# Optimization experiments

Measured on AMD Instinct MI355X. Metric: run time of the kernel, lower is better.

The kernel has to match this reference:

```python
import jax, jax.numpy as jnp
import numpy as np

D_MODEL = 768
N_HEADS = 12
HEAD_DIM = D_MODEL // N_HEADS
D_FF = 4 * D_MODEL
EPS = 1e-5


def setup_inputs() -> dict:
    key = jax.random.key(0)
    ks = jax.random.split(key, 16)
    s = 0.02
    x = jax.random.normal(ks[0], (2, 2048, D_MODEL), dtype=jnp.float32)
    wq = jax.random.normal(ks[1], (D_MODEL, D_MODEL), dtype=jnp.float32) * s
    bq = jnp.zeros((D_MODEL,), jnp.float32)
    wk = jax.random.normal(ks[2], (D_MODEL, D_MODEL), dtype=jnp.float32) * s
    bk = jnp.zeros((D_MODEL,), jnp.float32)
    wv = jax.random.normal(ks[3], (D_MODEL, D_MODEL), dtype=jnp.float32) * s
    bv = jnp.zeros((D_MODEL,), jnp.float32)
    wo = jax.random.normal(ks[4], (D_MODEL, D_MODEL), dtype=jnp.float32) * s
    bo = jnp.zeros((D_MODEL,), jnp.float32)
    w1 = jax.random.normal(ks[5], (D_MODEL, D_FF), dtype=jnp.float32) * s
    b1 = jnp.zeros((D_FF,), jnp.float32)
    w2 = jax.random.normal(ks[6], (D_FF, D_MODEL), dtype=jnp.float32) * s
    b2 = jnp.zeros((D_MODEL,), jnp.float32)
    ln1_g = jnp.ones((D_MODEL,), jnp.float32)
    ln1_b = jnp.zeros((D_MODEL,), jnp.float32)
    ln2_g = jnp.ones((D_MODEL,), jnp.float32)
    ln2_b = jnp.zeros((D_MODEL,), jnp.float32)
    return dict(x=x, wq=wq, bq=bq, wk=wk, bk=bk, wv=wv, bv=bv, wo=wo, bo=bo,
                w1=w1, b1=b1, w2=w2, b2=b2,
                ln1_g=ln1_g, ln1_b=ln1_b, ln2_g=ln2_g, ln2_b=ln2_b)


def _layernorm(x, g, b):
    mu = jnp.mean(x, axis=-1, keepdims=True)
    var = jnp.mean(jnp.square(x - mu), axis=-1, keepdims=True)
    return (x - mu) * jax.lax.rsqrt(var + EPS) * g + b


def _attention(x, wq, bq, wk, bk, wv, bv, wo, bo):
    B, S, D = x.shape
    def split_heads(t):  # [B,S,D] -> [B,H,S,Hd]
        return t.reshape(B, S, N_HEADS, HEAD_DIM).transpose(0, 2, 1, 3)
    q = split_heads(x @ wq + bq)
    k = split_heads(x @ wk + bk)
    v = split_heads(x @ wv + bv)
    scores = jnp.einsum('bhqd,bhkd->bhqk', q, k) / np.sqrt(HEAD_DIM).astype(np.float32)
    causal = jnp.tril(jnp.ones((S, S), dtype=bool))
    scores = jnp.where(causal, scores, -jnp.inf)
    weights = jax.nn.softmax(scores, axis=-1)
    attn = jnp.einsum('bhqk,bhkd->bhqd', weights, v)
    attn = attn.transpose(0, 2, 1, 3).reshape(B, S, D)
    return attn @ wo + bo


def reference(x, wq, bq, wk, bk, wv, bv, wo, bo, w1, b1, w2, b2,
              ln1_g, ln1_b, ln2_g, ln2_b):
    x = x + _attention(_layernorm(x, ln1_g, ln1_b), wq, bq, wk, bk, wv, bv, wo, bo)
    h = _layernorm(x, ln2_g, ln2_b)
    ff = jax.nn.relu(h @ w1 + b1) @ w2 + b2
    return x + ff
```

## Files before the change

### kernel.cpp

```cpp
#include <hip/hip_runtime.h>
#include <stdint.h>

typedef __bf16 bf16;
typedef float f32x4 __attribute__((ext_vector_type(4)));
typedef bf16 bf16x8 __attribute__((ext_vector_type(8)));
typedef bf16 bf16x4 __attribute__((ext_vector_type(4)));

#define MFMA16(a, b, c) __builtin_amdgcn_mfma_f32_16x16x32_bf16((a), (b), (c), 0, 0, 0)

static __device__ __forceinline__ void load_lds16(const bf16* g, bf16* l) {
  __builtin_amdgcn_global_load_lds(
      (const __attribute__((address_space(1))) void*)g,
      (__attribute__((address_space(3))) void*)l, 16, 0, 0);
}

static __device__ __forceinline__ void xcd_swz(int& bx, int& by, int& bz) {
  int gx = gridDim.x, gy = gridDim.y;
  int lin = blockIdx.x + gx * (blockIdx.y + gy * blockIdx.z);
  int nwg = gx * gy * gridDim.z;
  int nl = (lin & 7) * (nwg >> 3) + (lin >> 3);
  bx = nl % gx;
  int t = nl / gx;
  by = t % gy;
  bz = t / gy;
}

__global__ void __launch_bounds__(256) k_prep(
    const float* __restrict__ x, const float* __restrict__ ln1g,
    const float* __restrict__ ln1b, bf16* __restrict__ h1,
    const float* s0, const float* s1, const float* s2, const float* s3,
    const float* s4, const float* s5,
    bf16* d0, bf16* d1, bf16* d2, bf16* d3, bf16* d4, bf16* d5) {
  int t = blockIdx.x;
  int tid = threadIdx.x;
  if (t < 6912) {
    const float* src; bf16* dst; int R, C;
    if (t < 2304) {
      int z = t / 576; t -= z * 576;
      src = (z == 0) ? s0 : (z == 1) ? s1 : (z == 2) ? s2 : s3;
      dst = (z == 0) ? d0 : (z == 1) ? d1 : (z == 2) ? d2 : d3;
      R = 768; C = 768;
    } else if (t < 4608) {
      t -= 2304; src = s4; dst = d4; R = 768; C = 3072;
    } else {
      t -= 4608; src = s5; dst = d5; R = 3072; C = 768;
    }
    int tcn = C >> 5;
    int tr = t / tcn, tc = t % tcn;
    __shared__ float tile[32][33];
    int tx = tid & 31, ty = tid >> 5;
    for (int i = 0; i < 4; i++)
      tile[ty + i * 8][tx] = src[(size_t)(tr * 32 + ty + i * 8) * C + tc * 32 + tx];
    __syncthreads();
    for (int i = 0; i < 4; i++)
      dst[(size_t)(tc * 32 + ty + i * 8) * R + tr * 32 + tx] = (bf16)tile[tx][ty + i * 8];
  } else {
    int row = t - 6912;
    const float* rp = x + (size_t)row * 768;
    float v0 = rp[tid], v1 = rp[tid + 256], v2 = rp[tid + 512];
    float s = v0 + v1 + v2, sq = v0 * v0 + v1 * v1 + v2 * v2;
    for (int off = 1; off < 64; off <<= 1) {
      s += __shfl_xor(s, off, 64);
      sq += __shfl_xor(sq, off, 64);
    }
    __shared__ float ps[8];
    if ((tid & 63) == 0) { ps[tid >> 6] = s; ps[4 + (tid >> 6)] = sq; }
    __syncthreads();
    s = ps[0] + ps[1] + ps[2] + ps[3];
    sq = ps[4] + ps[5] + ps[6] + ps[7];
    float mu = s * (1.0f / 768.0f);
    float rstd = rsqrtf(sq * (1.0f / 768.0f) - mu * mu + 1e-5f);
    bf16* op = h1 + (size_t)row * 768;
    op[tid] = (bf16)((v0 - mu) * rstd * ln1g[tid] + ln1b[tid]);
    op[tid + 256] = (bf16)((v1 - mu) * rstd * ln1g[tid + 256] + ln1b[tid + 256]);
    op[tid + 512] = (bf16)((v2 - mu) * rstd * ln1g[tid + 512] + ln1b[tid + 512]);
  }
}

__global__ void __launch_bounds__(256) k_ln2_reduce(
    const float* __restrict__ p0, const float* __restrict__ p1,
    const float* __restrict__ x, const float* __restrict__ bo,
    const float* __restrict__ gam, const float* __restrict__ bet,
    float* __restrict__ x1, bf16* __restrict__ h2) {
  int row = blockIdx.x, tid = threadIdx.x;
  size_t base = (size_t)row * 768;
  float v0 = p0[base + tid] + p1[base + tid] + x[base + tid] + bo[tid];
  float v1 = p0[base + tid + 256] + p1[base + tid + 256] + x[base + tid + 256] + bo[tid + 256];
  float v2 = p0[base + tid + 512] + p1[base + tid + 512] + x[base + tid + 512] + bo[tid + 512];
  x1[base + tid] = v0; x1[base + tid + 256] = v1; x1[base + tid + 512] = v2;
  float s = v0 + v1 + v2, sq = v0 * v0 + v1 * v1 + v2 * v2;
  for (int off = 1; off < 64; off <<= 1) {
    s += __shfl_xor(s, off, 64);
    sq += __shfl_xor(sq, off, 64);
  }
  __shared__ float ps[8];
  if ((tid & 63) == 0) { ps[tid >> 6] = s; ps[4 + (tid >> 6)] = sq; }
  __syncthreads();
  s = ps[0] + ps[1] + ps[2] + ps[3];
  sq = ps[4] + ps[5] + ps[6] + ps[7];
  float mu = s * (1.0f / 768.0f);
  float rstd = rsqrtf(sq * (1.0f / 768.0f) - mu * mu + 1e-5f);
  bf16* op = h2 + base;
  op[tid] = (bf16)((v0 - mu) * rstd * gam[tid] + bet[tid]);
  op[tid + 256] = (bf16)((v1 - mu) * rstd * gam[tid + 256] + bet[tid + 256]);
  op[tid + 512] = (bf16)((v2 - mu) * rstd * gam[tid + 512] + bet[tid + 512]);
}

__global__ void __launch_bounds__(256) k_ff2_reduce(
    const float* __restrict__ f0, const float* __restrict__ f1,
    const float* __restrict__ x1, const float* __restrict__ b2,
    float* __restrict__ out) {
  size_t i = ((size_t)blockIdx.x * 256 + threadIdx.x) * 4;
  int col = (int)(i % 768);
  f32x4 v = *(const f32x4*)(x1 + i);
  f32x4 b = *(const f32x4*)(b2 + col);
  f32x4 a0 = *(const f32x4*)(f0 + i), a1 = *(const f32x4*)(f1 + i);
  *(f32x4*)(out + i) = v + b + a0 + a1;
}

template <int MT>
static __device__ __forceinline__ void gemm_core(
    const bf16* __restrict__ A, int lda, const bf16* __restrict__ Bt, int ldb,
    int Kc, int m0, int n0, bf16* As, bf16* Bs, f32x4 acc[MT][4]) {
  int tid = threadIdx.x, w = tid >> 6, lane = tid & 63, quad = lane >> 4, l15 = lane & 15;
  int wr = w >> 1, wc = w & 1;
  int srow = lane >> 2;
  int sk = (((lane & 3) ^ ((srow >> 1) & 3)) * 8);
  int rsw = ((l15 >> 1) & 3);
  const int ABUF = MT * 32 * 32;
  const int BBUF = 128 * 32;

  auto stage = [&](int k0, int buf) {
    bf16* Ab = As + buf * ABUF;
    bf16* Bb = Bs + buf * BBUF;
    if (MT == 4) {
      for (int c = 0; c < 2; c++) {
        int seg = w * 2 + c;
        load_lds16(A + (size_t)(m0 + seg * 16 + srow) * lda + k0 + sk, Ab + seg * 512);
      }
    } else {
      load_lds16(A + (size_t)(m0 + w * 16 + srow) * lda + k0 + sk, Ab + w * 512);
    }
    for (int c = 0; c < 2; c++) {
      int seg = w * 2 + c;
      load_lds16(Bt + (size_t)(n0 + seg * 16 + srow) * ldb + k0 + sk, Bb + seg * 512);
    }
  };

  stage(0, 0);
  stage(32, 1);
  int cur = 0;
  for (int k0 = 0; k0 < Kc; k0 += 32) {
    if (k0 + 32 < Kc) {
      if (MT == 4) asm volatile("s_waitcnt vmcnt(4)" ::: "memory");
      else         asm volatile("s_waitcnt vmcnt(3)" ::: "memory");
    } else {
      asm volatile("s_waitcnt vmcnt(0)" ::: "memory");
    }
    __builtin_amdgcn_s_barrier();
    __builtin_amdgcn_sched_barrier(0);
    if (k0 + 64 < Kc) {
      int nb = cur + 2; if (nb >= 3) nb -= 3;
      stage(k0 + 64, nb);
    }
    const bf16* Ab = As + cur * ABUF;
    const bf16* Bb = Bs + cur * BBUF;
    bf16x8 af[MT], bfr[4];
    for (int mi = 0; mi < MT; mi++)
      af[mi] = *(const bf16x8*)(Ab + (wr * (MT * 16) + mi * 16 + l15) * 32 + ((quad ^ rsw) * 8));
    for (int ni = 0; ni < 4; ni++)
      bfr[ni] = *(const bf16x8*)(Bb + (wc * 64 + ni * 16 + l15) * 32 + ((quad ^ rsw) * 8));
    for (int mi = 0; mi < MT; mi++)
      for (int ni = 0; ni < 4; ni++)
        acc[mi][ni] = MFMA16(af[mi], bfr[ni], acc[mi][ni]);
    cur = cur + 1; if (cur >= 3) cur -= 3;
  }
}

template <int MT>
static __device__ __forceinline__ void gemm_core64(
    const bf16* __restrict__ A, int lda, const bf16* __restrict__ Bt, int ldb,
    int Kc, int m0, int n0, bf16* As, bf16* Bs, f32x4 acc[MT][4]) {
  int tid = threadIdx.x, w = tid >> 6, lane = tid & 63, quad = lane >> 4, l15 = lane & 15;
  int wr = w >> 1, wc = w & 1;
  int srow = lane >> 2;
  int sk = (((lane & 3) ^ ((srow >> 1) & 3)) * 8);
  int rsw = ((l15 >> 1) & 3);
  const int ASUB = MT * 32 * 32;
  const int BSUB = 128 * 32;
  const int ABUF = 2 * ASUB;
  const int BBUF = 2 * BSUB;

  auto stage = [&](int k0, int buf) {
    bf16* Ab = As + buf * ABUF;
    bf16* Bb = Bs + buf * BBUF;
    for (int h = 0; h < 2; h++) {
      if (MT == 4) {
        for (int c = 0; c < 2; c++) {
          int seg = w * 2 + c;
          load_lds16(A + (size_t)(m0 + seg * 16 + srow) * lda + k0 + h * 32 + sk,
                     Ab + h * ASUB + seg * 512);
        }
      } else {
        load_lds16(A + (size_t)(m0 + w * 16 + srow) * lda + k0 + h * 32 + sk,
                   Ab + h * ASUB + w * 512);
      }
      for (int c = 0; c < 2; c++) {
        int seg = w * 2 + c;
        load_lds16(Bt + (size_t)(n0 + seg * 16 + srow) * ldb + k0 + h * 32 + sk,
                   Bb + h * BSUB + seg * 512);
      }
    }
  };

  stage(0, 0);
  int cur = 0;
  for (int k0 = 0; k0 < Kc; k0 += 64) {
    __syncthreads();
    if (k0 + 64 < Kc) stage(k0 + 64, cur ^ 1);
    const bf16* Ab = As + cur * ABUF;
    const bf16* Bb = Bs + cur * BBUF;
    for (int h = 0; h < 2; h++) {
      bf16x8 af[MT], bfr[4];
      for (int mi = 0; mi < MT; mi++)
        af[mi] = *(const bf16x8*)(Ab + h * ASUB +
                 (wr * (MT * 16) + mi * 16 + l15) * 32 + ((quad ^ rsw) * 8));
      for (int ni = 0; ni < 4; ni++)
        bfr[ni] = *(const bf16x8*)(Bb + h * BSUB +
                  (wc * 64 + ni * 16 + l15) * 32 + ((quad ^ rsw) * 8));
      for (int mi = 0; mi < MT; mi++)
        for (int ni = 0; ni < 4; ni++)
          acc[mi][ni] = MFMA16(af[mi], bfr[ni], acc[mi][ni]);
    }
    cur ^= 1;
  }
}

template <int MT>
__global__ void __launch_bounds__(256, 3) k_gemm(
    const bf16* __restrict__ A, const bf16* __restrict__ Bt,
    const float* __restrict__ bias, bf16* __restrict__ outp, int K_, int N_) {
  __shared__ __align__(16) bf16 As[3 * MT * 32 * 32];
  __shared__ __align__(16) bf16 Bs[3 * 128 * 32];
  int bx, by, bz;
  xcd_swz(bx, by, bz);
  int m0 = by * (MT * 32), n0 = bx * 128;
  f32x4 acc[MT][4] = {};
  gemm_core<MT>(A, K_, Bt, K_, K_, m0, n0, As, Bs, acc);
  int tid = threadIdx.x, w = tid >> 6, lane = tid & 63, quad = lane >> 4, l15 = lane & 15;
  int wr = w >> 1, wc = w & 1;
  float bv[4];
  for (int ni = 0; ni < 4; ni++) bv[ni] = bias[n0 + wc * 64 + ni * 16 + l15];
  for (int mi = 0; mi < MT; mi++) {
    int mb = m0 + wr * (MT * 16) + mi * 16 + quad * 4;
    for (int ni = 0; ni < 4; ni++) {
      int n = n0 + wc * 64 + ni * 16 + l15;
      for (int r = 0; r < 4; r++) {
        float val = acc[mi][ni][r] + bv[ni];
        outp[(size_t)(mb + r) * N_ + n] = (bf16)fmaxf(val, 0.0f);
      }
    }
  }
}

__global__ void __launch_bounds__(256, 3) k_gemm_split64(
    const bf16* __restrict__ A, const bf16* __restrict__ Bt,
    float* __restrict__ f0, float* __restrict__ f1, int K_, int Kc, int N_) {
  __shared__ __align__(16) bf16 As[2 * 2 * 2 * 32 * 32];
  __shared__ __align__(16) bf16 Bs[2 * 2 * 128 * 32];
  int bx, by, bz;
  xcd_swz(bx, by, bz);
  float* outp = (bz == 0) ? f0 : f1;
  int m0 = by * 64, n0 = bx * 128;
  f32x4 acc[2][4] = {};
  gemm_core64<2>(A + (size_t)bz * Kc, K_, Bt + (size_t)bz * Kc, K_, Kc, m0, n0, As, Bs, acc);
  int tid = threadIdx.x, w = tid >> 6, lane = tid & 63, quad = lane >> 4, l15 = lane & 15;
  int wr = w >> 1, wc = w & 1;
  for (int mi = 0; mi < 2; mi++) {
    int mb = m0 + wr * 32 + mi * 16 + quad * 4;
    for (int ni = 0; ni < 4; ni++) {
      int n = n0 + wc * 64 + ni * 16 + l15;
      for (int r = 0; r < 4; r++)
        outp[(size_t)(mb + r) * N_ + n] = acc[mi][ni][r];
    }
  }
}

__global__ void __launch_bounds__(256, 3) k_gemm_qkv64(
    const bf16* __restrict__ h1, const bf16* __restrict__ wqT,
    const bf16* __restrict__ wkT, const bf16* __restrict__ wvT,
    const float* __restrict__ bq, const float* __restrict__ bk,
    const float* __restrict__ bv, bf16* __restrict__ qb,
    bf16* __restrict__ kb, bf16* __restrict__ vtb) {
  __shared__ __align__(16) bf16 As[2 * 2 * 2 * 32 * 32];
  __shared__ __align__(16) bf16 Bs[2 * 2 * 128 * 32];
  int bx, by, bz;
  xcd_swz(bx, by, bz);
  int z = bz;
  const bf16* Bt = (z == 0) ? wqT : (z == 1) ? wkT : wvT;
  const float* bias = (z == 0) ? bq : (z == 1) ? bk : bv;
  int m0 = by * 64, n0 = bx * 128;
  f32x4 acc[2][4] = {};
  gemm_core64<2>(h1, 768, Bt, 768, 768, m0, n0, As, Bs, acc);
  int tid = threadIdx.x, w = tid >> 6, lane = tid & 63, quad = lane >> 4, l15 = lane & 15;
  int wr = w >> 1, wc = w & 1;
  float bvv[4];
  for (int ni = 0; ni < 4; ni++) bvv[ni] = bias[n0 + wc * 64 + ni * 16 + l15];
  for (int mi = 0; mi < 2; mi++) {
    int mb = m0 + wr * 32 + mi * 16 + quad * 4;
    int b = mb >> 11, s0_ = mb & 2047;
    for (int ni = 0; ni < 4; ni++) {
      int n = n0 + wc * 64 + ni * 16 + l15;
      int h = n >> 6, hd = n & 63;
      if (z < 2) {
        bf16* outp = (z == 0) ? qb : kb;
        size_t base = (size_t)(b * 12 + h) * 2048 * 64;
        for (int r = 0; r < 4; r++)
          outp[base + (size_t)(s0_ + r) * 64 + hd] = (bf16)(acc[mi][ni][r] + bvv[ni]);
      } else {
        bf16x4 pk;
        for (int r = 0; r < 4; r++) pk[r] = (bf16)(acc[mi][ni][r] + bvv[ni]);
        *(bf16x4*)(vtb + (((size_t)(b * 12 + h) * 64 + hd) * 2048 + s0_)) = pk;
      }
    }
  }
}

__global__ void __launch_bounds__(256, 2) k_attn(
    const bf16* __restrict__ qb, const bf16* __restrict__ kb,
    const bf16* __restrict__ vtb, bf16* __restrict__ out) {
  __shared__ __align__(16) bf16 Ks[2 * 128 * 64];
  __shared__ __align__(16) bf16 Vs[2 * 64 * 128];
  __shared__ __align__(16) bf16 Ps[4][16 * 128];
  int qt = 31 - (blockIdx.x / 24);
  int bh = blockIdx.x % 24;
  int q0 = qt * 64;
  int tid = threadIdx.x, w = tid >> 6, lane = tid & 63, quad = lane >> 4, l15 = lane & 15;
  const bf16* qbase = qb + (size_t)bh * 2048 * 64;
  const bf16* kbase = kb + (size_t)bh * 2048 * 64;
  const bf16* vbase = vtb + (size_t)bh * 64 * 2048;

  bf16x8 qf[2];
  for (int ds = 0; ds < 2; ds++)
    qf[ds] = *(const bf16x8*)(qbase + (size_t)(q0 + w * 16 + l15) * 64 + ds * 32 + quad * 8);

  bf16 one_ = (bf16)1.0f;
  bf16x8 ones8 = {one_, one_, one_, one_, one_, one_, one_, one_};

  f32x4 o[4] = {};
  f32x4 lacc = {};

  auto stageKV = [&](int k0, int buf) {
    int rsub = lane >> 3, c8 = lane & 7;
    bf16* Kb = Ks + buf * (128 * 64);
    for (int c = 0; c < 4; c++) {
      int seg = c * 4 + w;
      int row = seg * 8 + rsub;
      load_lds16(kbase + (size_t)(k0 + row) * 64 + ((c8 ^ (row & 7)) * 8), Kb + seg * 512);
    }
    int rsub2 = lane >> 4, c16 = lane & 15;
    bf16* Vb = Vs + buf * (64 * 128);
    for (int c = 0; c < 4; c++) {
      int seg = c * 4 + w;
      int row = seg * 4 + rsub2;
      load_lds16(vbase + (size_t)row * 2048 + k0 + ((c16 ^ (row & 15)) * 8), Vb + seg * 512);
    }
  };

  const float C2 = 0.18033688011112042f;
  int nkt = (qt >> 1) + 1;
  stageKV(0, 0);
  int cur = 0;
  for (int kt = 0; kt < nkt; kt++) {
    int k0 = kt * 128;
    __syncthreads();
    if (kt + 1 < nkt) stageKV(k0 + 128, cur ^ 1);
    const bf16* Kb = Ks + cur * (128 * 64);
    const bf16* Vb = Vs + cur * (64 * 128);

    f32x4 sc[8] = {};
    __builtin_amdgcn_s_setprio(1);
    for (int kj = 0; kj < 8; kj++) {
      int krow = kj * 16 + l15;
      for (int ds = 0; ds < 2; ds++) {
        bf16x8 kf = *(const bf16x8*)(Kb + krow * 64 + (((ds * 4 + quad) ^ (krow & 7)) * 8));
        sc[kj] = MFMA16(qf[ds], kf, sc[kj]);
      }
    }
    __builtin_amdgcn_s_setprio(0);
    if (kt == nkt - 1) {
      int qg = q0 + w * 16 + quad * 4;
      for (int kj = 0; kj < 8; kj++) {
        int kg = k0 + kj * 16 + l15;
        for (int r = 0; r < 4; r++)
          if (kg > qg + r) sc[kj][r] = -3.0e38f;
      }
    }
    for (int kj = 0; kj < 8; kj++)
      for (int r = 0; r < 4; r++)
        sc[kj][r] = exp2f(sc[kj][r] * C2);
    for (int kj = 0; kj < 8; kj++) {
      int colb = kj * 16 + l15;
      int chb = colb >> 3, cin = colb & 7;
      for (int r = 0; r < 4; r++) {
        int prow = quad * 4 + r;
        Ps[w][prow * 128 + ((chb ^ prow) * 8) + cin] = (bf16)sc[kj][r];
      }
    }
    __builtin_amdgcn_s_setprio(1);
    for (int ks = 0; ks < 4; ks++) {
      int prow = l15;
      bf16x8 pf = *(const bf16x8*)(&Ps[w][prow * 128 + (((ks * 4 + quad) ^ prow) * 8)]);
      lacc = MFMA16(pf, ones8, lacc);
      for (int dj = 0; dj < 4; dj++) {
        int vrow = dj * 16 + l15;
        bf16x8 vf = *(const bf16x8*)(Vb + vrow * 128 + (((ks * 4 + quad) ^ (vrow & 15)) * 8));
        o[dj] = MFMA16(pf, vf, o[dj]);
      }
    }
    __builtin_amdgcn_s_setprio(0);
    cur ^= 1;
  }
  int b = bh / 12, h = bh % 12;
  f32x4 rl;
  for (int r = 0; r < 4; r++) rl[r] = 1.0f / lacc[r];
  int srow = q0 + w * 16 + quad * 4;
  for (int dj = 0; dj < 4; dj++) {
    int d = h * 64 + dj * 16 + l15;
    for (int r = 0; r < 4; r++)
      out[(size_t)(b * 2048 + srow + r) * 768 + d] = (bf16)(o[dj][r] * rl[r]);
  }
}

extern "C" void kernel_launch(void* const* d_in, const int* in_sizes, int n_in,
                              void* d_out, int out_size, void* d_ws, size_t ws_size,
                              hipStream_t stream) {
  const float* x    = (const float*)d_in[0];
  const float* wq   = (const float*)d_in[1];
  const float* bq   = (const float*)d_in[2];
  const float* wk   = (const float*)d_in[3];
  const float* bk   = (const float*)d_in[4];
  const float* wv   = (const float*)d_in[5];
  const float* bv   = (const float*)d_in[6];
  const float* wo   = (const float*)d_in[7];
  const float* bo   = (const float*)d_in[8];
  const float* w1   = (const float*)d_in[9];
  const float* b1   = (const float*)d_in[10];
  const float* w2   = (const float*)d_in[11];
  const float* b2   = (const float*)d_in[12];
  const float* ln1g = (const float*)d_in[13];
  const float* ln1b = (const float*)d_in[14];
  const float* ln2g = (const float*)d_in[15];
  const float* ln2b = (const float*)d_in[16];

  char* p = (char*)d_ws;
  bf16* wqT = (bf16*)p; p += (size_t)768 * 768 * 2;
  bf16* wkT = (bf16*)p; p += (size_t)768 * 768 * 2;
  bf16* wvT = (bf16*)p; p += (size_t)768 * 768 * 2;
  bf16* woT = (bf16*)p; p += (size_t)768 * 768 * 2;
  bf16* w1T = (bf16*)p; p += (size_t)768 * 3072 * 2;
  bf16* w2T = (bf16*)p; p += (size_t)768 * 3072 * 2;
  bf16* h1   = (bf16*)p; p += (size_t)4096 * 768 * 2;
  bf16* qbuf = (bf16*)p; p += (size_t)4096 * 768 * 2;
  bf16* kbuf = (bf16*)p; p += (size_t)4096 * 768 * 2;
  bf16* vtb  = (bf16*)p; p += (size_t)4096 * 768 * 2;
  bf16* att  = (bf16*)p; p += (size_t)4096 * 768 * 2;
  float* x1  = (float*)p; p += (size_t)4096 * 768 * 4;
  bf16* h2   = (bf16*)p; p += (size_t)4096 * 768 * 2;
  bf16* ffm  = (bf16*)p; p += (size_t)4096 * 3072 * 2;
  float* p0  = (float*)p; p += (size_t)4096 * 768 * 4;
  float* p1  = (float*)p; p += (size_t)4096 * 768 * 4;
  float* f0 = (float*)h1;
  float* f1 = (float*)kbuf;

  k_prep<<<dim3(11008), dim3(256), 0, stream>>>(
      x, ln1g, ln1b, h1, wq, wk, wv, wo, w1, w2, wqT, wkT, wvT, woT, w1T, w2T);
  k_gemm_qkv64<<<dim3(6, 64, 3), dim3(256), 0, stream>>>(
      h1, wqT, wkT, wvT, bq, bk, bv, qbuf, kbuf, vtb);
  k_attn<<<dim3(768), dim3(256), 0, stream>>>(qbuf, kbuf, vtb, att);
  k_gemm_split64<<<dim3(6, 64, 2), dim3(256), 0, stream>>>(
      att, woT, p0, p1, 768, 384, 768);
  k_ln2_reduce<<<dim3(4096), dim3(256), 0, stream>>>(
      p0, p1, x, bo, ln2g, ln2b, x1, h2);
  k_gemm<4><<<dim3(24, 32), dim3(256), 0, stream>>>(
      h2, w1T, b1, ffm, 768, 3072);
  k_gemm_split64<<<dim3(6, 64, 2), dim3(256), 0, stream>>>(
      ffm, w2T, f0, f1, 3072, 1536, 768);
  k_ff2_reduce<<<dim3(3072), dim3(256), 0, stream>>>(
      f0, f1, x1, b2, (float*)d_out);
}
```

Baseline: 265.8 us.

## Fold residual into Wo GEMM, prescale Q, retile FF1 GEMM to 64-row

Moves the residual x and bias bo addition into the epilogue of the first split-K Wo GEMM partition, so the LN2 reduce kernel reads two fp32 arrays instead of four. Folds the softmax scale constant into Q when the QKV GEMM writes it, which removes one multiply per score in attention. Replaces the FF1 GEMM, which used a 128-row tile with a three-stage 32-K pipeline, with a 64-row tile using the double-buffered 64-K core. That doubles the grid and cuts per-block work. Rounding Q to bf16 after scaling changes numerics slightly.

After: 276.2 us. 1.04x slower.

```diff
diff --git a/kernel.cpp b/kernel.cpp
--- a/kernel.cpp
+++ b/kernel.cpp
@@ -79,14 +79,13 @@
 
 __global__ void __launch_bounds__(256) k_ln2_reduce(
     const float* __restrict__ p0, const float* __restrict__ p1,
-    const float* __restrict__ x, const float* __restrict__ bo,
     const float* __restrict__ gam, const float* __restrict__ bet,
     float* __restrict__ x1, bf16* __restrict__ h2) {
   int row = blockIdx.x, tid = threadIdx.x;
   size_t base = (size_t)row * 768;
-  float v0 = p0[base + tid] + p1[base + tid] + x[base + tid] + bo[tid];
-  float v1 = p0[base + tid + 256] + p1[base + tid + 256] + x[base + tid + 256] + bo[tid + 256];
-  float v2 = p0[base + tid + 512] + p1[base + tid + 512] + x[base + tid + 512] + bo[tid + 512];
+  float v0 = p0[base + tid] + p1[base + tid];
+  float v1 = p0[base + tid + 256] + p1[base + tid + 256];
+  float v2 = p0[base + tid + 512] + p1[base + tid + 512];
   x1[base + tid] = v0; x1[base + tid + 256] = v1; x1[base + tid + 512] = v2;
   float s = v0 + v1 + v2, sq = v0 * v0 + v1 * v1 + v2 * v2;
   for (int off = 1; off < 64; off <<= 1) {
@@ -118,75 +117,15 @@
   *(f32x4*)(out + i) = v + b + a0 + a1;
 }
 
-template <int MT>
-static __device__ __forceinline__ void gemm_core(
+static __device__ __forceinline__ void gemm_core64(
     const bf16* __restrict__ A, int lda, const bf16* __restrict__ Bt, int ldb,
-    int Kc, int m0, int n0, bf16* As, bf16* Bs, f32x4 acc[MT][4]) {
+    int Kc, int m0, int n0, bf16* As, bf16* Bs, f32x4 acc[2][4]) {
   int tid = threadIdx.x, w = tid >> 6, lane = tid & 63, quad = lane >> 4, l15 = lane & 15;
   int wr = w >> 1, wc = w & 1;
   int srow = lane >> 2;
   int sk = (((lane & 3) ^ ((srow >> 1) & 3)) * 8);
   int rsw = ((l15 >> 1) & 3);
-  const int ABUF = MT * 32 * 32;
-  const int BBUF = 128 * 32;
-
-  auto stage = [&](int k0, int buf) {
-    bf16* Ab = As + buf * ABUF;
-    bf16* Bb = Bs + buf * BBUF;
-    if (MT == 4) {
-      for (int c = 0; c < 2; c++) {
-        int seg = w * 2 + c;
-        load_lds16(A + (size_t)(m0 + seg * 16 + srow) * lda + k0 + sk, Ab + seg * 512);
-      }
-    } else {
-      load_lds16(A + (size_t)(m0 + w * 16 + srow) * lda + k0 + sk, Ab + w * 512);
-    }
-    for (int c = 0; c < 2; c++) {
-      int seg = w * 2 + c;
-      load_lds16(Bt + (size_t)(n0 + seg * 16 + srow) * ldb + k0 + sk, Bb + seg * 512);
-    }
-  };
-
-  stage(0, 0);
-  stage(32, 1);
-  int cur = 0;
-  for (int k0 = 0; k0 < Kc; k0 += 32) {
-    if (k0 + 32 < Kc) {
-      if (MT == 4) asm volatile("s_waitcnt vmcnt(4)" ::: "memory");
-      else         asm volatile("s_waitcnt vmcnt(3)" ::: "memory");
-    } else {
-      asm volatile("s_waitcnt vmcnt(0)" ::: "memory");
-    }
-    __builtin_amdgcn_s_barrier();
-    __builtin_amdgcn_sched_barrier(0);
-    if (k0 + 64 < Kc) {
-      int nb = cur + 2; if (nb >= 3) nb -= 3;
-      stage(k0 + 64, nb);
-    }
-    const bf16* Ab = As + cur * ABUF;
-    const bf16* Bb = Bs + cur * BBUF;
-    bf16x8 af[MT], bfr[4];
-    for (int mi = 0; mi < MT; mi++)
-      af[mi] = *(const bf16x8*)(Ab + (wr * (MT * 16) + mi * 16 + l15) * 32 + ((quad ^ rsw) * 8));
-    for (int ni = 0; ni < 4; ni++)
-      bfr[ni] = *(const bf16x8*)(Bb + (wc * 64 + ni * 16 + l15) * 32 + ((quad ^ rsw) * 8));
-    for (int mi = 0; mi < MT; mi++)
-      for (int ni = 0; ni < 4; ni++)
-        acc[mi][ni] = MFMA16(af[mi], bfr[ni], acc[mi][ni]);
-    cur = cur + 1; if (cur >= 3) cur -= 3;
-  }
-}
-
-template <int MT>
-static __device__ __forceinline__ void gemm_core64(
-    const bf16* __restrict__ A, int lda, const bf16* __restrict__ Bt, int ldb,
-    int Kc, int m0, int n0, bf16* As, bf16* Bs, f32x4 acc[MT][4]) {
-  int tid = threadIdx.x, w = tid >> 6, lane = tid & 63, quad = lane >> 4, l15 = lane & 15;
-  int wr = w >> 1, wc = w & 1;
-  int srow = lane >> 2;
-  int sk = (((lane & 3) ^ ((srow >> 1) & 3)) * 8);
-  int rsw = ((l15 >> 1) & 3);
-  const int ASUB = MT * 32 * 32;
+  const int ASUB = 2 * 32 * 32;
   const int BSUB = 128 * 32;
   const int ABUF = 2 * ASUB;
   const int BBUF = 2 * BSUB;
@@ -195,16 +134,8 @@
     bf16* Ab = As + buf * ABUF;
     bf16* Bb = Bs + buf * BBUF;
     for (int h = 0; h < 2; h++) {
-      if (MT == 4) {
-        for (int c = 0; c < 2; c++) {
-          int seg = w * 2 + c;
-          load_lds16(A + (size_t)(m0 + seg * 16 + srow) * lda + k0 + h * 32 + sk,
-                     Ab + h * ASUB + seg * 512);
-        }
-      } else {
-        load_lds16(A + (size_t)(m0 + w * 16 + srow) * lda + k0 + h * 32 + sk,
-                   Ab + h * ASUB + w * 512);
-      }
+      load_lds16(A + (size_t)(m0 + w * 16 + srow) * lda + k0 + h * 32 + sk,
+                 Ab + h * ASUB + w * 512);
       for (int c = 0; c < 2; c++) {
         int seg = w * 2 + c;
         load_lds16(Bt + (size_t)(n0 + seg * 16 + srow) * ldb + k0 + h * 32 + sk,
@@ -221,14 +152,14 @@
     const bf16* Ab = As + cur * ABUF;
     const bf16* Bb = Bs + cur * BBUF;
     for (int h = 0; h < 2; h++) {
-      bf16x8 af[MT], bfr[4];
-      for (int mi = 0; mi < MT; mi++)
+      bf16x8 af[2], bfr[4];
+      for (int mi = 0; mi < 2; mi++)
         af[mi] = *(const bf16x8*)(Ab + h * ASUB +
-                 (wr * (MT * 16) + mi * 16 + l15) * 32 + ((quad ^ rsw) * 8));
+                 (wr * 32 + mi * 16 + l15) * 32 + ((quad ^ rsw) * 8));
       for (int ni = 0; ni < 4; ni++)
         bfr[ni] = *(const bf16x8*)(Bb + h * BSUB +
                   (wc * 64 + ni * 16 + l15) * 32 + ((quad ^ rsw) * 8));
-      for (int mi = 0; mi < MT; mi++)
+      for (int mi = 0; mi < 2; mi++)
         for (int ni = 0; ni < 4; ni++)
           acc[mi][ni] = MFMA16(af[mi], bfr[ni], acc[mi][ni]);
     }
@@ -236,23 +167,22 @@
   }
 }
 
-template <int MT>
-__global__ void __launch_bounds__(256, 3) k_gemm(
+__global__ void __launch_bounds__(256, 3) k_gemm64(
     const bf16* __restrict__ A, const bf16* __restrict__ Bt,
     const float* __restrict__ bias, bf16* __restrict__ outp, int K_, int N_) {
-  __shared__ __align__(16) bf16 As[3 * MT * 32 * 32];
-  __shared__ __align__(16) bf16 Bs[3 * 128 * 32];
+  __shared__ __align__(16) bf16 As[2 * 2 * 2 * 32 * 32];
+  __shared__ __align__(16) bf16 Bs[2 * 2 * 128 * 32];
   int bx, by, bz;
   xcd_swz(bx, by, bz);
-  int m0 = by * (MT * 32), n0 = bx * 128;
-  f32x4 acc[MT][4] = {};
-  gemm_core<MT>(A, K_, Bt, K_, K_, m0, n0, As, Bs, acc);
+  int m0 = by * 64, n0 = bx * 128;
+  f32x4 acc[2][4] = {};
+  gemm_core64(A, K_, Bt, K_, K_, m0, n0, As, Bs, acc);
   int tid = threadIdx.x, w = tid >> 6, lane = tid & 63, quad = lane >> 4, l15 = lane & 15;
   int wr = w >> 1, wc = w & 1;
   float bv[4];
   for (int ni = 0; ni < 4; ni++) bv[ni] = bias[n0 + wc * 64 + ni * 16 + l15];
-  for (int mi = 0; mi < MT; mi++) {
-    int mb = m0 + wr * (MT * 16) + mi * 16 + quad * 4;
+  for (int mi = 0; mi < 2; mi++) {
+    int mb = m0 + wr * 32 + mi * 16 + quad * 4;
     for (int ni = 0; ni < 4; ni++) {
       int n = n0 + wc * 64 + ni * 16 + l15;
       for (int r = 0; r < 4; r++) {
@@ -265,7 +195,9 @@
 
 __global__ void __launch_bounds__(256, 3) k_gemm_split64(
     const bf16* __restrict__ A, const bf16* __restrict__ Bt,
-    float* __restrict__ f0, float* __restrict__ f1, int K_, int Kc, int N_) {
+    float* __restrict__ f0, float* __restrict__ f1,
+    const float* __restrict__ xadd, const float* __restrict__ badd,
+    int K_, int Kc, int N_) {
   __shared__ __align__(16) bf16 As[2 * 2 * 2 * 32 * 32];
   __shared__ __align__(16) bf16 Bs[2 * 2 * 128 * 32];
   int bx, by, bz;
@@ -273,15 +205,19 @@
   float* outp = (bz == 0) ? f0 : f1;
   int m0 = by * 64, n0 = bx * 128;
   f32x4 acc[2][4] = {};
-  gemm_core64<2>(A + (size_t)bz * Kc, K_, Bt + (size_t)bz * Kc, K_, Kc, m0, n0, As, Bs, acc);
+  gemm_core64(A + (size_t)bz * Kc, K_, Bt + (size_t)bz * Kc, K_, Kc, m0, n0, As, Bs, acc);
   int tid = threadIdx.x, w = tid >> 6, lane = tid & 63, quad = lane >> 4, l15 = lane & 15;
   int wr = w >> 1, wc = w & 1;
+  bool fold = (bz == 0) && (xadd != nullptr);
   for (int mi = 0; mi < 2; mi++) {
     int mb = m0 + wr * 32 + mi * 16 + quad * 4;
     for (int ni = 0; ni < 4; ni++) {
       int n = n0 + wc * 64 + ni * 16 + l15;
-      for (int r = 0; r < 4; r++)
-        outp[(size_t)(mb + r) * N_ + n] = acc[mi][ni][r];
+      for (int r = 0; r < 4; r++) {
+        float val = acc[mi][ni][r];
+        if (fold) val += xadd[(size_t)(mb + r) * N_ + n] + badd[n];
+        outp[(size_t)(mb + r) * N_ + n] = val;
+      }
     }
   }
 }
@@ -301,9 +237,11 @@
   const float* bias = (z == 0) ? bq : (z == 1) ? bk : bv;
   int m0 = by * 64, n0 = bx * 128;
   f32x4 acc[2][4] = {};
-  gemm_core64<2>(h1, 768, Bt, 768, 768, m0, n0, As, Bs, acc);
+  gemm_core64(h1, 768, Bt, 768, 768, m0, n0, As, Bs, acc);
   int tid = threadIdx.x, w = tid >> 6, lane = tid & 63, quad = lane >> 4, l15 = lane & 15;
   int wr = w >> 1, wc = w & 1;
+  const float C2 = 0.18033688011112042f;
+  float qs = (z == 0) ? C2 : 1.0f;
   float bvv[4];
   for (int ni = 0; ni < 4; ni++) bvv[ni] = bias[n0 + wc * 64 + ni * 16 + l15];
   for (int mi = 0; mi < 2; mi++) {
@@ -316,7 +254,7 @@
         bf16* outp = (z == 0) ? qb : kb;
         size_t base = (size_t)(b * 12 + h) * 2048 * 64;
         for (int r = 0; r < 4; r++)
-          outp[base + (size_t)(s0_ + r) * 64 + hd] = (bf16)(acc[mi][ni][r] + bvv[ni]);
+          outp[base + (size_t)(s0_ + r) * 64 + hd] = (bf16)((acc[mi][ni][r] + bvv[ni]) * qs);
       } else {
         bf16x4 pk;
         for (int r = 0; r < 4; r++) pk[r] = (bf16)(acc[mi][ni][r] + bvv[ni]);
@@ -367,7 +305,6 @@
     }
   };
 
-  const float C2 = 0.18033688011112042f;
   int nkt = (qt >> 1) + 1;
   stageKV(0, 0);
   int cur = 0;
@@ -398,7 +335,7 @@
     }
     for (int kj = 0; kj < 8; kj++)
       for (int r = 0; r < 4; r++)
-        sc[kj][r] = exp2f(sc[kj][r] * C2);
+        sc[kj][r] = exp2f(sc[kj][r]);
     for (int kj = 0; kj < 8; kj++) {
       int colb = kj * 16 + l15;
       int chb = colb >> 3, cin = colb & 7;
@@ -479,13 +416,13 @@
       h1, wqT, wkT, wvT, bq, bk, bv, qbuf, kbuf, vtb);
   k_attn<<<dim3(768), dim3(256), 0, stream>>>(qbuf, kbuf, vtb, att);
   k_gemm_split64<<<dim3(6, 64, 2), dim3(256), 0, stream>>>(
-      att, woT, p0, p1, 768, 384, 768);
+      att, woT, p0, p1, x, bo, 768, 384, 768);
   k_ln2_reduce<<<dim3(4096), dim3(256), 0, stream>>>(
-      p0, p1, x, bo, ln2g, ln2b, x1, h2);
-  k_gemm<4><<<dim3(24, 32), dim3(256), 0, stream>>>(
+      p0, p1, ln2g, ln2b, x1, h2);
+  k_gemm64<<<dim3(24, 64), dim3(256), 0, stream>>>(
       h2, w1T, b1, ffm, 768, 3072);
   k_gemm_split64<<<dim3(6, 64, 2), dim3(256), 0, stream>>>(
-      ffm, w2T, f0, f1, 3072, 1536, 768);
+      ffm, w2T, f0, f1, nullptr, nullptr, 3072, 1536, 768);
   k_ff2_reduce<<<dim3(3072), dim3(256), 0, stream>>>(
       f0, f1, x1, b2, (float*)d_out);
 }
```
